# Performance work log

Measured on AMD Instinct MI355X. Metric: run time of the kernel, lower is better.

## Reference

```python
import jax, jax.numpy as jnp
import numpy as np

RANK = 4
ALPHA = 4.0
SCALE = ALPHA / RANK


def setup_inputs() -> dict:
    key = jax.random.key(0)
    k1, k2, k3, k4 = jax.random.split(key, 4)
    B, S, H = 4, 2048, 2048
    NH, HD = 16, 128
    x = jax.random.normal(k1, (B, S, H), dtype=jnp.float32)
    W_orig = jax.random.normal(k2, (H, NH, HD), dtype=jnp.float32) * (1.0 / np.sqrt(H))
    A_kernel = jax.random.normal(k3, (H, RANK), dtype=jnp.float32) * (1.0 / RANK)
    # B kernel is zero-init in the module; use small randn so the LoRA path is exercised
    B_kernel = jax.random.normal(k4, (RANK, NH, HD), dtype=jnp.float32) * 0.02
    return {"x": x, "W_orig": W_orig, "A_kernel": A_kernel, "B_kernel": B_kernel}


def reference(x, W_orig, A_kernel, B_kernel):
    # original layer: EinsumDense 'abc,cde->abde'  [B,S,H] x [H,NH,HD] -> [B,S,NH,HD]
    original_output = jnp.einsum('bsc,chd->bshd', x, W_orig)
    # LoRA path: Dense to rank, then EinsumDense back up, scaled
    ax = x @ A_kernel                                   # [B,S,r]
    lora_output = jnp.einsum('bsr,rhd->bshd', ax, B_kernel) * SCALE
    return original_output + lora_output
```

## Files before the change

kernel.cpp:

```cpp
#include <hip/hip_runtime.h>
#include <hip/hip_bf16.h>
#include <cstdint>


using bf16 = __hip_bfloat16;
typedef __attribute__((ext_vector_type(8))) __bf16 bf16x8;
typedef __attribute__((ext_vector_type(4))) float f32x4;

constexpr int Mdim = 8192;
constexpr int Ndim = 2048;
constexpr int Kdim = 2048;
constexpr float SCALE = 1.0f;

constexpr int BM = 128, BN = 128, BK = 64;

__device__ __forceinline__ void gload_lds16(const void* g, void* l) {
  __builtin_amdgcn_global_load_lds(
      (const __attribute__((address_space(1))) uint32_t*)g,
      (__attribute__((address_space(3))) uint32_t*)l,
      16, 0, 0);
}

__global__ void cvt_x(const float4* __restrict__ X, uint16_t* __restrict__ Xb) {
  const int i = blockIdx.x * blockDim.x + threadIdx.x;
  float4 a = X[i * 2 + 0];
  float4 b = X[i * 2 + 1];
  uint16_t o[8];
  o[0] = __bfloat16_as_ushort(__float2bfloat16(a.x));
  o[1] = __bfloat16_as_ushort(__float2bfloat16(a.y));
  o[2] = __bfloat16_as_ushort(__float2bfloat16(a.z));
  o[3] = __bfloat16_as_ushort(__float2bfloat16(a.w));
  o[4] = __bfloat16_as_ushort(__float2bfloat16(b.x));
  o[5] = __bfloat16_as_ushort(__float2bfloat16(b.y));
  o[6] = __bfloat16_as_ushort(__float2bfloat16(b.z));
  o[7] = __bfloat16_as_ushort(__float2bfloat16(b.w));
  *reinterpret_cast<uint4*>(Xb + (size_t)i * 8) = *reinterpret_cast<uint4*>(o);
}

__global__ void prep_wt(const float* __restrict__ W, const float* __restrict__ A,
                        const float* __restrict__ Bk, uint16_t* __restrict__ Wt) {
  __shared__ float tile[64][65];
  const int tx = threadIdx.x & 63;
  const int ty = threadIdx.x >> 6;
  const int n0 = blockIdx.x * 64, k0 = blockIdx.y * 64;

  const int n = n0 + tx;
  const float b0 = Bk[0 * Ndim + n];
  const float b1 = Bk[1 * Ndim + n];
  const float b2 = Bk[2 * Ndim + n];
  const float b3 = Bk[3 * Ndim + n];

  for (int i = ty; i < 64; i += 4) {
    const int k = k0 + i;
    float w = W[(size_t)k * Ndim + n];
    w += SCALE * (A[k * 4 + 0] * b0 + A[k * 4 + 1] * b1 +
                  A[k * 4 + 2] * b2 + A[k * 4 + 3] * b3);
    tile[tx][i] = w;
  }
  __syncthreads();
  for (int i = ty; i < 64; i += 4) {
    Wt[(size_t)(n0 + i) * Kdim + (k0 + tx)] =
        __bfloat16_as_ushort(__float2bfloat16(tile[i][tx]));
  }
}

__global__ void gemm_bt(const uint16_t* __restrict__ X,
                        const uint16_t* __restrict__ Wt,
                        float* __restrict__ out) {
  __shared__ uint16_t As[BM * BK];
  __shared__ uint16_t Bs[BN * BK];

  const int t = threadIdx.x;
  const int wave = t >> 6, lane = t & 63;
  const int m0 = blockIdx.y * BM, n0 = blockIdx.x * BN;

  const int wm = wave & 1, wn = wave >> 1;
  const int l15 = lane & 15, kg = lane >> 4;
  const int sw = l15 & 7;

  const int r8 = lane >> 3;
  const int gc = (lane & 7) ^ r8;
  const uint16_t* Ag = X + (size_t)m0 * Kdim;
  const uint16_t* Bg = Wt + (size_t)n0 * Kdim;

  f32x4 acc[4][4] = {};

  for (int kt = 0; kt < Kdim; kt += BK) {
#pragma unroll
    for (int c = 0; c < 4; ++c) {
      const int ch = wave * 4 + c;
      const int row = ch * 8 + r8;
      gload_lds16(Ag + (size_t)row * Kdim + kt + gc * 8, &As[ch * 512]);
      gload_lds16(Bg + (size_t)row * Kdim + kt + gc * 8, &Bs[ch * 512]);
    }
    __syncthreads();

#pragma unroll
    for (int s = 0; s < 2; ++s) {
      bf16x8 af[4], bfr[4];
      const int p = (s * 4 + kg) ^ sw;
#pragma unroll
      for (int i = 0; i < 4; ++i) {
        const int ra = wm * 64 + i * 16 + l15;
        const int rb = wn * 64 + i * 16 + l15;
        af[i]  = *reinterpret_cast<const bf16x8*>(&As[ra * BK + p * 8]);
        bfr[i] = *reinterpret_cast<const bf16x8*>(&Bs[rb * BK + p * 8]);
      }
#pragma unroll
      for (int i = 0; i < 4; ++i)
#pragma unroll
        for (int j = 0; j < 4; ++j)
          acc[i][j] = __builtin_amdgcn_mfma_f32_16x16x32_bf16(af[i], bfr[j], acc[i][j], 0, 0, 0);
    }
    __syncthreads();
  }

#pragma unroll
  for (int i = 0; i < 4; ++i) {
    const int m_base = m0 + wm * 64 + i * 16 + kg * 4;
#pragma unroll
    for (int j = 0; j < 4; ++j) {
      const int n = n0 + wn * 64 + j * 16 + l15;
#pragma unroll
      for (int r = 0; r < 4; ++r) {
        out[(size_t)(m_base + r) * Ndim + n] = acc[i][j][r];
      }
    }
  }
}

extern "C" void kernel_launch(void* const* d_in, const int* in_sizes, int n_in,
                              void* d_out, int out_size, void* d_ws, size_t ws_size,
                              hipStream_t stream) {
  const float* x  = (const float*)d_in[0];
  const float* W  = (const float*)d_in[1];
  const float* A  = (const float*)d_in[2];
  const float* Bk = (const float*)d_in[3];
  float* out = (float*)d_out;

  uint16_t* Xb = (uint16_t*)d_ws;
  uint16_t* Wt = (uint16_t*)((char*)d_ws + (size_t)Mdim * Kdim * 2);

  const int n_elem = Mdim * Kdim;
  cvt_x<<<n_elem / (256 * 8), 256, 0, stream>>>((const float4*)x, Xb);

  dim3 g1(Ndim / 64, Kdim / 64);
  prep_wt<<<g1, 256, 0, stream>>>(W, A, Bk, Wt);

  dim3 g2(Ndim / BN, Mdim / BM);
  gemm_bt<<<g2, 256, 0, stream>>>(Xb, Wt, out);
}
```

Measured before the change: 202.1 us.

## Fuse fp32-to-bf16 conversion of x into GEMM tile loading

Removes the separate cvt_x pass and loads fp32 x directly in the GEMM, converting to bf16 in registers and writing swizzled tiles into LDS. This drops the round trip through a bf16 workspace copy of x. In exchange, each GEMM block now reads fp32 x (twice the bytes), and since 16 N-tiles each reread the same rows, total A traffic from L2/HBM grows. The A loads are also synchronous register loads instead of direct-to-LDS loads. Output stores become nontemporal.

```diff
diff --git a/kernel.cpp b/kernel.cpp
--- a/kernel.cpp
+++ b/kernel.cpp
@@ -19,22 +19,6 @@
       (const __attribute__((address_space(1))) uint32_t*)g,
       (__attribute__((address_space(3))) uint32_t*)l,
       16, 0, 0);
-}
-
-__global__ void cvt_x(const float4* __restrict__ X, uint16_t* __restrict__ Xb) {
-  const int i = blockIdx.x * blockDim.x + threadIdx.x;
-  float4 a = X[i * 2 + 0];
-  float4 b = X[i * 2 + 1];
-  uint16_t o[8];
-  o[0] = __bfloat16_as_ushort(__float2bfloat16(a.x));
-  o[1] = __bfloat16_as_ushort(__float2bfloat16(a.y));
-  o[2] = __bfloat16_as_ushort(__float2bfloat16(a.z));
-  o[3] = __bfloat16_as_ushort(__float2bfloat16(a.w));
-  o[4] = __bfloat16_as_ushort(__float2bfloat16(b.x));
-  o[5] = __bfloat16_as_ushort(__float2bfloat16(b.y));
-  o[6] = __bfloat16_as_ushort(__float2bfloat16(b.z));
-  o[7] = __bfloat16_as_ushort(__float2bfloat16(b.w));
-  *reinterpret_cast<uint4*>(Xb + (size_t)i * 8) = *reinterpret_cast<uint4*>(o);
 }
 
 __global__ void prep_wt(const float* __restrict__ W, const float* __restrict__ A,
@@ -64,9 +48,9 @@
   }
 }
 
-__global__ void gemm_bt(const uint16_t* __restrict__ X,
-                        const uint16_t* __restrict__ Wt,
-                        float* __restrict__ out) {
+__global__ void gemm_xf32(const float* __restrict__ X,
+                          const uint16_t* __restrict__ Wt,
+                          float* __restrict__ out) {
   __shared__ uint16_t As[BM * BK];
   __shared__ uint16_t Bs[BN * BK];
 
@@ -79,9 +63,13 @@
   const int sw = l15 & 7;
 
   const int r8 = lane >> 3;
-  const int gc = (lane & 7) ^ r8;
-  const uint16_t* Ag = X + (size_t)m0 * Kdim;
+  const int gcB = (lane & 7) ^ r8;
   const uint16_t* Bg = Wt + (size_t)n0 * Kdim;
+
+  const int g4 = lane >> 4;
+  const int cA = l15 >> 1;
+  const int halfA = l15 & 1;
+  const float* Xg = X + (size_t)m0 * Kdim;
 
   f32x4 acc[4][4] = {};
 
@@ -90,8 +78,25 @@
     for (int c = 0; c < 4; ++c) {
       const int ch = wave * 4 + c;
       const int row = ch * 8 + r8;
-      gload_lds16(Ag + (size_t)row * Kdim + kt + gc * 8, &As[ch * 512]);
-      gload_lds16(Bg + (size_t)row * Kdim + kt + gc * 8, &Bs[ch * 512]);
+      gload_lds16(Bg + (size_t)row * Kdim + kt + gcB * 8, &Bs[ch * 512]);
+    }
+    float4 av[8];
+#pragma unroll
+    for (int i = 0; i < 8; ++i) {
+      const int row = wave * 32 + i * 4 + g4;
+      av[i] = *reinterpret_cast<const float4*>(Xg + (size_t)row * Kdim + kt + l15 * 4);
+    }
+#pragma unroll
+    for (int i = 0; i < 8; ++i) {
+      const int row = wave * 32 + i * 4 + g4;
+      const int p = cA ^ (row & 7);
+      ushort4 o;
+      o.x = __bfloat16_as_ushort(__float2bfloat16(av[i].x));
+      o.y = __bfloat16_as_ushort(__float2bfloat16(av[i].y));
+      o.z = __bfloat16_as_ushort(__float2bfloat16(av[i].z));
+      o.w = __bfloat16_as_ushort(__float2bfloat16(av[i].w));
+      *reinterpret_cast<uint2*>(&As[row * BK + p * 8 + halfA * 4]) =
+          *reinterpret_cast<uint2*>(&o);
     }
     __syncthreads();
 
@@ -123,7 +128,8 @@
       const int n = n0 + wn * 64 + j * 16 + l15;
 #pragma unroll
       for (int r = 0; r < 4; ++r) {
-        out[(size_t)(m_base + r) * Ndim + n] = acc[i][j][r];
+        __builtin_nontemporal_store(acc[i][j][r],
+                                    &out[(size_t)(m_base + r) * Ndim + n]);
       }
     }
   }
@@ -138,15 +144,11 @@
   const float* Bk = (const float*)d_in[3];
   float* out = (float*)d_out;
 
-  uint16_t* Xb = (uint16_t*)d_ws;
-  uint16_t* Wt = (uint16_t*)((char*)d_ws + (size_t)Mdim * Kdim * 2);
-
-  const int n_elem = Mdim * Kdim;
-  cvt_x<<<n_elem / (256 * 8), 256, 0, stream>>>((const float4*)x, Xb);
+  uint16_t* Wt = (uint16_t*)d_ws;
 
   dim3 g1(Ndim / 64, Kdim / 64);
   prep_wt<<<g1, 256, 0, stream>>>(W, A, Bk, Wt);
 
   dim3 g2(Ndim / BN, Mdim / BM);
-  gemm_bt<<<g2, 256, 0, stream>>>(Xb, Wt, out);
+  gemm_xf32<<<g2, 256, 0, stream>>>(x, Wt, out);
 }
```

After: 232.7 us. 15.1% more time.
